# Optimization experiments

Hardware: AMD Instinct MI355X
Metric: run time of the kernel (lower is better)

Reference implementation:

```python
import jax, jax.numpy as jnp
import numpy as np

B, N, M, E = 2, 16384, 16384, 49152
W_CHAMFER, W_EDGE = 1.0, 0.1


def setup_inputs() -> dict:
    key = jax.random.key(0)
    k1, k2, k3 = jax.random.split(key, 3)
    pred_verts = jax.random.normal(k1, (B, N, 3), dtype=jnp.float32)
    target_verts = jax.random.normal(k2, (B, M, 3), dtype=jnp.float32)
    edges = jax.random.randint(k3, (E, 2), 0, N, dtype=jnp.int64)
    return {"pred_verts": pred_verts, "target_verts": target_verts, "edges": edges}


def reference(pred_verts, target_verts, edges):
    # --- Chamfer distance (torch.cdist + bidirectional min) ---
    # Squared-distance expansion avoids materializing the B x N x M x 3 diff tensor.
    p2 = jnp.sum(pred_verts * pred_verts, axis=-1)            # [B, N]
    t2 = jnp.sum(target_verts * target_verts, axis=-1)        # [B, M]
    cross = jnp.einsum('bnd,bmd->bnm', pred_verts, target_verts)  # [B, N, M]
    d2 = p2[:, :, None] + t2[:, None, :] - 2.0 * cross
    dist = jnp.sqrt(jnp.maximum(d2, 0.0))                     # [B, N, M]
    c_loss = jnp.mean(jnp.min(dist, axis=2)) + jnp.mean(jnp.min(dist, axis=1))

    # --- Edge-length variance regularization (vectorized over batch) ---
    v1 = pred_verts[:, edges[:, 0]]                           # [B, E, 3]
    v2 = pred_verts[:, edges[:, 1]]                           # [B, E, 3]
    edge_lengths = jnp.linalg.norm(v1 - v2, axis=-1)          # [B, E]
    # torch.var defaults to unbiased (ddof=1); mean over batch == sum/B
    e_loss = jnp.mean(jnp.var(edge_lengths, axis=1, ddof=1))

    total_loss = W_CHAMFER * c_loss + W_EDGE * e_loss
    return (total_loss, c_loss, e_loss)
```

## Files before the change

### kernel.cpp

```cpp
#include <hip/hip_runtime.h>
#include <float.h>

#define B_SZ 2
#define N_SZ 16384
#define E_SZ 49152

#define TPB 512
#define WAVES (TPB / 64)
#define ROWS_PER_BLOCK 128
#define NTILES (N_SZ / 32)
#define TILES_PER_CG (NTILES / 4)

#define CH_BLOCKS_PER_DIR (B_SZ * N_SZ / ROWS_PER_BLOCK)
#define CH_BLOCKS (2 * CH_BLOCKS_PER_DIR)
#define EDGE_BLOCKS (B_SZ * E_SZ / TPB)

#define PLANE_BYTES (N_SZ * 16)
#define BATCH_FRAG_BYTES (2 * PLANE_BYTES)
#define DIR_FRAG_BYTES (B_SZ * BATCH_FRAG_BYTES)
#define SUMS_OFF (2 * DIR_FRAG_BYTES)

typedef short short8 __attribute__((ext_vector_type(8)));
typedef float f32x16 __attribute__((ext_vector_type(16)));

__device__ inline short f2bf(float f) {
    unsigned u = __float_as_uint(f);
    unsigned r = (u + 0x7fffu + ((u >> 16) & 1u)) >> 16;
    return (short)r;
}
__device__ inline float bf2f(short s) {
    return __uint_as_float(((unsigned)(unsigned short)s) << 16);
}

__global__ __launch_bounds__(TPB) void prep(const float* __restrict__ pred,
                                            const float* __restrict__ tgt,
                                            char* __restrict__ ws) {
    int idx = blockIdx.x * TPB + threadIdx.x;
    double* sums = (double*)(ws + SUMS_OFF);
    if (blockIdx.x == 0 && threadIdx.x < 6) sums[threadIdx.x] = 0.0;

    const bool isTgt = idx < B_SZ * N_SZ;
    int row = isTgt ? idx : idx - B_SZ * N_SZ;
    int batch = row >> 14, pt = row & (N_SZ - 1);
    const float* src = (isTgt ? tgt : pred) + (size_t)row * 3;
    char* base = ws + (isTgt ? 0 : DIR_FRAG_BYTES) + (size_t)batch * BATCH_FRAG_BYTES;

    float tx = src[0], ty = src[1], tz = src[2];
    short hx = f2bf(tx), hy = f2bf(ty), hz = f2bf(tz);
    short lx = f2bf(tx - bf2f(hx)), ly = f2bf(ty - bf2f(hy)), lz = f2bf(tz - bf2f(hz));
    float t2 = fmaf(tx, tx, fmaf(ty, ty, tz * tz));
    short t2h = f2bf(t2), t2l = f2bf(t2 - bf2f(t2h));
    const short one = 0x3f80;

    *(short8*)(base + (size_t)pt * 16) = (short8){hx, hy, hz, hx, hy, hz, one, one};
    *(short8*)(base + PLANE_BYTES + (size_t)pt * 16) =
        (short8){lx, ly, lz, t2h, t2l, 0, 0, 0};
}

__global__ __launch_bounds__(TPB, 2) void main_kernel(
    const float* __restrict__ pred, const float* __restrict__ tgt,
    const int* __restrict__ edges, char* __restrict__ ws)
{
    __shared__ float wred[WAVES], wred2[WAVES];
    __shared__ int rowMin[ROWS_PER_BLOCK];
    double* sums = (double*)(ws + SUMS_OFF);
    const int lane = threadIdx.x & 63;
    const int wv = threadIdx.x >> 6;
    const int t = threadIdx.x;

    if (blockIdx.x < CH_BLOCKS) {
        const int dir = blockIdx.x >> 8;
        const int xb = blockIdx.x & 255;
        const int batch = xb >> 7;
        const int rowInB = (xb & 127) * ROWS_PER_BLOCK;
        const float* P = dir ? tgt : pred;
        const char* fragBase = ws + (size_t)dir * DIR_FRAG_BYTES
                                  + (size_t)batch * BATCH_FRAG_BYTES;
        const int bl = lane & 31;
        const int half = lane >> 5;
        const int rp = wv & 1;
        const int cg = wv >> 1;

        if (t < ROWS_PER_BLOCK) rowMin[t] = 0x7f7fffff;

        const short one = 0x3f80;
        short8 af[2];
        #pragma unroll
        for (int j = 0; j < 2; j++) {
            int r = batch * N_SZ + rowInB + rp * 64 + j * 32 + bl;
            const float* p = P + (size_t)r * 3;
            float px = p[0], py = p[1], pz = p[2];
            float ax = -2.f * px, ay = -2.f * py, az = -2.f * pz;
            short ahx = f2bf(ax), ahy = f2bf(ay), ahz = f2bf(az);
            short alx = f2bf(ax - bf2f(ahx)), aly = f2bf(ay - bf2f(ahy)),
                  alz = f2bf(az - bf2f(ahz));
            float p2 = fmaf(px, px, fmaf(py, py, pz * pz));
            short p2h = f2bf(p2), p2l = f2bf(p2 - bf2f(p2h));
            af[j] = half == 0
                ? (short8){ahx, ahy, ahz, alx, aly, alz, p2h, p2l}
                : (short8){ahx, ahy, ahz, one, one, 0, 0, 0};
        }

        float acc0[16], acc1[16];
        #pragma unroll
        for (int e = 0; e < 16; e++) { acc0[e] = FLT_MAX; acc1[e] = FLT_MAX; }
        const f32x16 zc = {0.f, 0.f, 0.f, 0.f, 0.f, 0.f, 0.f, 0.f,
                           0.f, 0.f, 0.f, 0.f, 0.f, 0.f, 0.f, 0.f};

        const char* bbase = fragBase + (size_t)half * PLANE_BYTES
                                     + (size_t)bl * 16;
        const int tbase = cg * TILES_PER_CG;
        auto ldb = [&](int tc) {
            return *(const short8*)(bbase + (size_t)tc * 512);
        };

        #define DOPAIR(X0, X1)                                                 \
            do {                                                               \
                f32x16 r0 = __builtin_amdgcn_mfma_f32_32x32x16_bf16(af[0], X0, zc, 0, 0, 0); \
                f32x16 r1 = __builtin_amdgcn_mfma_f32_32x32x16_bf16(af[0], X1, zc, 0, 0, 0); \
                _Pragma("unroll")                                              \
                for (int e = 0; e < 16; e++)                                   \
                    acc0[e] = fminf(fminf(r0[e], r1[e]), acc0[e]);             \
                f32x16 s0 = __builtin_amdgcn_mfma_f32_32x32x16_bf16(af[1], X0, zc, 0, 0, 0); \
                f32x16 s1 = __builtin_amdgcn_mfma_f32_32x32x16_bf16(af[1], X1, zc, 0, 0, 0); \
                _Pragma("unroll")                                              \
                for (int e = 0; e < 16; e++)                                   \
                    acc1[e] = fminf(fminf(s0[e], s1[e]), acc1[e]);             \
            } while (0)

        short8 b0 = ldb(tbase + 0), b1 = ldb(tbase + 1);
        short8 b2 = ldb(tbase + 2), b3 = ldb(tbase + 3);
        __syncthreads();

        #pragma unroll 1
        for (int i = 0; i < TILES_PER_CG / 4; i++) {
            int pf = (i < TILES_PER_CG / 4 - 1) ? tbase + 4 * (i + 1) : tbase;
            {
                short8 x0 = b0, x1 = b1;
                b0 = ldb(pf + 0); b1 = ldb(pf + 1);
                DOPAIR(x0, x1);
            }
            {
                short8 x0 = b2, x1 = b3;
                b2 = ldb(pf + 2); b3 = ldb(pf + 3);
                DOPAIR(x0, x1);
            }
        }

        #pragma unroll
        for (int j = 0; j < 2; j++) {
            #pragma unroll
            for (int e = 0; e < 16; e++) {
                float v = (j == 0) ? acc0[e] : acc1[e];
                v = fminf(v, __shfl_xor(v, 1));
                v = fminf(v, __shfl_xor(v, 2));
                v = fminf(v, __shfl_xor(v, 4));
                v = fminf(v, __shfl_xor(v, 8));
                v = fminf(v, __shfl_xor(v, 16));
                if (bl == 0) {
                    int row = rp * 64 + j * 32 + (e & 3) + 8 * (e >> 2) + 4 * half;
                    atomicMin(&rowMin[row], __float_as_int(fmaxf(v, 0.f)));
                }
            }
        }
        __syncthreads();

        if (t < ROWS_PER_BLOCK) {
            float s = sqrtf(__int_as_float(rowMin[t]));
            #pragma unroll
            for (int o = 32; o > 0; o >>= 1) s += __shfl_down(s, o, 64);
            if (lane == 0) wred[wv] = s;
        }
        __syncthreads();
        if (t == 0) atomicAdd(&sums[dir], (double)(wred[0] + wred[1]));
    } else {
        int idx = (blockIdx.x - CH_BLOCKS) * TPB + threadIdx.x;
        int b = idx >= E_SZ;
        int e = idx - b * E_SZ;
        int2 ee = ((const int2*)edges)[e];
        const float* p0 = pred + ((size_t)b * N_SZ + (size_t)ee.x) * 3;
        const float* p1 = pred + ((size_t)b * N_SZ + (size_t)ee.y) * 3;
        float dx = p0[0] - p1[0], dy = p0[1] - p1[1], dz = p0[2] - p1[2];
        float len = sqrtf(dx * dx + dy * dy + dz * dz);
        float s = len, q = len * len;
        for (int o = 32; o > 0; o >>= 1) {
            s += __shfl_down(s, o, 64);
            q += __shfl_down(q, o, 64);
        }
        if (lane == 0) { wred[wv] = s; wred2[wv] = q; }
        __syncthreads();
        if (threadIdx.x == 0) {
            float ts = 0.f, tq = 0.f;
            #pragma unroll
            for (int w = 0; w < WAVES; w++) { ts += wred[w]; tq += wred2[w]; }
            atomicAdd(&sums[2 + 2 * b], (double)ts);
            atomicAdd(&sums[3 + 2 * b], (double)tq);
        }
    }
}

__global__ void final_kernel(const char* __restrict__ ws, float* __restrict__ out) {
    const double* sums = (const double*)(ws + SUMS_OFF);
    double c = sums[0] / (double)(B_SZ * N_SZ) + sums[1] / (double)(B_SZ * N_SZ);
    double e = 0.0;
    #pragma unroll
    for (int b = 0; b < B_SZ; b++) {
        double s = sums[2 + 2 * b], q = sums[3 + 2 * b];
        e += (q - s * s / (double)E_SZ) / (double)(E_SZ - 1);
    }
    e *= (1.0 / B_SZ);
    double tot = 1.0 * c + 0.1 * e;
    out[0] = (float)tot;
    out[1] = (float)c;
    out[2] = (float)e;
}

extern "C" void kernel_launch(void* const* d_in, const int* in_sizes, int n_in,
                              void* d_out, int out_size, void* d_ws, size_t ws_size,
                              hipStream_t stream) {
    const float* pred = (const float*)d_in[0];
    const float* tgt  = (const float*)d_in[1];
    const int* edges  = (const int*)d_in[2];
    float* out = (float*)d_out;
    char* ws = (char*)d_ws;

    prep<<<dim3((2 * B_SZ * N_SZ) / TPB), TPB, 0, stream>>>(pred, tgt, ws);

    main_kernel<<<dim3(CH_BLOCKS + EDGE_BLOCKS), TPB, 0, stream>>>(
        pred, tgt, edges, ws);

    final_kernel<<<dim3(1), dim3(1), 0, stream>>>(ws, out);
}
```

Before: 104.0 us.

## Compute both chamfer directions from one distance pass with column-min reduction

Instead of running the distance matrix twice (pred→tgt and tgt→pred), each block now computes the pred×tgt tile once and derives both the row minima and the column minima. Column minima are reduced in a 64KB LDS array per block and then merged into a global array with atomicMin. A new colsum kernel takes sqrt of each column minimum and sums them. This halves the MFMA work, but adds per-tile shuffle and LDS atomic traffic, a large LDS footprint that may reduce occupancy, and global atomic merges.

```diff
diff --git a/kernel.cpp b/kernel.cpp
--- a/kernel.cpp
+++ b/kernel.cpp
@@ -11,13 +11,13 @@
 #define NTILES (N_SZ / 32)
 #define TILES_PER_CG (NTILES / 4)
 
-#define CH_BLOCKS_PER_DIR (B_SZ * N_SZ / ROWS_PER_BLOCK)
-#define CH_BLOCKS (2 * CH_BLOCKS_PER_DIR)
+#define CH_BLOCKS (B_SZ * N_SZ / ROWS_PER_BLOCK)
 #define EDGE_BLOCKS (B_SZ * E_SZ / TPB)
 
 #define PLANE_BYTES (N_SZ * 16)
 #define BATCH_FRAG_BYTES (2 * PLANE_BYTES)
 #define DIR_FRAG_BYTES (B_SZ * BATCH_FRAG_BYTES)
+#define COLMIN_OFF DIR_FRAG_BYTES
 #define SUMS_OFF (2 * DIR_FRAG_BYTES)
 
 typedef short short8 __attribute__((ext_vector_type(8)));
@@ -32,18 +32,16 @@
     return __uint_as_float(((unsigned)(unsigned short)s) << 16);
 }
 
-__global__ __launch_bounds__(TPB) void prep(const float* __restrict__ pred,
-                                            const float* __restrict__ tgt,
+__global__ __launch_bounds__(TPB) void prep(const float* __restrict__ tgt,
                                             char* __restrict__ ws) {
     int idx = blockIdx.x * TPB + threadIdx.x;
     double* sums = (double*)(ws + SUMS_OFF);
     if (blockIdx.x == 0 && threadIdx.x < 6) sums[threadIdx.x] = 0.0;
-
-    const bool isTgt = idx < B_SZ * N_SZ;
-    int row = isTgt ? idx : idx - B_SZ * N_SZ;
-    int batch = row >> 14, pt = row & (N_SZ - 1);
-    const float* src = (isTgt ? tgt : pred) + (size_t)row * 3;
-    char* base = ws + (isTgt ? 0 : DIR_FRAG_BYTES) + (size_t)batch * BATCH_FRAG_BYTES;
+    ((int*)(ws + COLMIN_OFF))[idx] = 0x7f7fffff;
+
+    int batch = idx >> 14, pt = idx & (N_SZ - 1);
+    const float* src = tgt + (size_t)idx * 3;
+    char* base = ws + (size_t)batch * BATCH_FRAG_BYTES;
 
     float tx = src[0], ty = src[1], tz = src[2];
     short hx = f2bf(tx), hy = f2bf(ty), hz = f2bf(tz);
@@ -61,6 +59,7 @@
     const float* __restrict__ pred, const float* __restrict__ tgt,
     const int* __restrict__ edges, char* __restrict__ ws)
 {
+    __shared__ int colLds[N_SZ];
     __shared__ float wred[WAVES], wred2[WAVES];
     __shared__ int rowMin[ROWS_PER_BLOCK];
     double* sums = (double*)(ws + SUMS_OFF);
@@ -69,18 +68,15 @@
     const int t = threadIdx.x;
 
     if (blockIdx.x < CH_BLOCKS) {
-        const int dir = blockIdx.x >> 8;
-        const int xb = blockIdx.x & 255;
-        const int batch = xb >> 7;
-        const int rowInB = (xb & 127) * ROWS_PER_BLOCK;
-        const float* P = dir ? tgt : pred;
-        const char* fragBase = ws + (size_t)dir * DIR_FRAG_BYTES
-                                  + (size_t)batch * BATCH_FRAG_BYTES;
+        const int batch = blockIdx.x >> 7;
+        const int rowInB = (blockIdx.x & 127) * ROWS_PER_BLOCK;
+        const char* fragBase = ws + (size_t)batch * BATCH_FRAG_BYTES;
         const int bl = lane & 31;
         const int half = lane >> 5;
         const int rp = wv & 1;
         const int cg = wv >> 1;
 
+        for (int k = t; k < N_SZ; k += TPB) colLds[k] = 0x7f7fffff;
         if (t < ROWS_PER_BLOCK) rowMin[t] = 0x7f7fffff;
 
         const short one = 0x3f80;
@@ -88,7 +84,7 @@
         #pragma unroll
         for (int j = 0; j < 2; j++) {
             int r = batch * N_SZ + rowInB + rp * 64 + j * 32 + bl;
-            const float* p = P + (size_t)r * 3;
+            const float* p = pred + (size_t)r * 3;
             float px = p[0], py = p[1], pz = p[2];
             float ax = -2.f * px, ay = -2.f * py, az = -2.f * pz;
             short ahx = f2bf(ax), ahy = f2bf(ay), ahz = f2bf(az);
@@ -113,20 +109,31 @@
         auto ldb = [&](int tc) {
             return *(const short8*)(bbase + (size_t)tc * 512);
         };
-
-        #define DOPAIR(X0, X1)                                                 \
-            do {                                                               \
-                f32x16 r0 = __builtin_amdgcn_mfma_f32_32x32x16_bf16(af[0], X0, zc, 0, 0, 0); \
-                f32x16 r1 = __builtin_amdgcn_mfma_f32_32x32x16_bf16(af[0], X1, zc, 0, 0, 0); \
-                _Pragma("unroll")                                              \
-                for (int e = 0; e < 16; e++)                                   \
-                    acc0[e] = fminf(fminf(r0[e], r1[e]), acc0[e]);             \
-                f32x16 s0 = __builtin_amdgcn_mfma_f32_32x32x16_bf16(af[1], X0, zc, 0, 0, 0); \
-                f32x16 s1 = __builtin_amdgcn_mfma_f32_32x32x16_bf16(af[1], X1, zc, 0, 0, 0); \
-                _Pragma("unroll")                                              \
-                for (int e = 0; e < 16; e++)                                   \
-                    acc1[e] = fminf(fminf(s0[e], s1[e]), acc1[e]);             \
-            } while (0)
+        auto coltree = [&](const f32x16& r, const f32x16& s, int tc) {
+            float m[8];
+            #pragma unroll
+            for (int e = 0; e < 8; e++)
+                m[e] = fminf(fminf(r[e], r[e + 8]), fminf(s[e], s[e + 8]));
+            float cv = fminf(fminf(fminf(m[0], m[1]), fminf(m[2], m[3])),
+                             fminf(fminf(m[4], m[5]), fminf(m[6], m[7])));
+            cv = fminf(cv, __shfl_xor(cv, 32));
+            if (half == 0)
+                atomicMin(&colLds[tc * 32 + bl], __float_as_int(fmaxf(cv, 0.f)));
+        };
+        auto dopair = [&](short8 x0, short8 x1, int tc0) {
+            f32x16 r0 = __builtin_amdgcn_mfma_f32_32x32x16_bf16(af[0], x0, zc, 0, 0, 0);
+            f32x16 r1 = __builtin_amdgcn_mfma_f32_32x32x16_bf16(af[0], x1, zc, 0, 0, 0);
+            f32x16 s0 = __builtin_amdgcn_mfma_f32_32x32x16_bf16(af[1], x0, zc, 0, 0, 0);
+            f32x16 s1 = __builtin_amdgcn_mfma_f32_32x32x16_bf16(af[1], x1, zc, 0, 0, 0);
+            #pragma unroll
+            for (int e = 0; e < 16; e++)
+                acc0[e] = fminf(fminf(r0[e], r1[e]), acc0[e]);
+            #pragma unroll
+            for (int e = 0; e < 16; e++)
+                acc1[e] = fminf(fminf(s0[e], s1[e]), acc1[e]);
+            coltree(r0, s0, tc0);
+            coltree(r1, s1, tc0 + 1);
+        };
 
         short8 b0 = ldb(tbase + 0), b1 = ldb(tbase + 1);
         short8 b2 = ldb(tbase + 2), b3 = ldb(tbase + 3);
@@ -134,16 +141,17 @@
 
         #pragma unroll 1
         for (int i = 0; i < TILES_PER_CG / 4; i++) {
-            int pf = (i < TILES_PER_CG / 4 - 1) ? tbase + 4 * (i + 1) : tbase;
+            int tc = tbase + 4 * i;
+            int pf = (i < TILES_PER_CG / 4 - 1) ? tc + 4 : tbase;
             {
                 short8 x0 = b0, x1 = b1;
                 b0 = ldb(pf + 0); b1 = ldb(pf + 1);
-                DOPAIR(x0, x1);
+                dopair(x0, x1, tc);
             }
             {
                 short8 x0 = b2, x1 = b3;
                 b2 = ldb(pf + 2); b3 = ldb(pf + 3);
-                DOPAIR(x0, x1);
+                dopair(x0, x1, tc + 2);
             }
         }
 
@@ -172,7 +180,13 @@
             if (lane == 0) wred[wv] = s;
         }
         __syncthreads();
-        if (t == 0) atomicAdd(&sums[dir], (double)(wred[0] + wred[1]));
+        if (t == 0) atomicAdd(&sums[0], (double)(wred[0] + wred[1]));
+
+        int* colG = (int*)(ws + COLMIN_OFF) + batch * N_SZ;
+        for (int k = t; k < N_SZ; k += TPB) {
+            int v = colLds[k];
+            if (v < colG[k]) atomicMin(&colG[k], v);
+        }
     } else {
         int idx = (blockIdx.x - CH_BLOCKS) * TPB + threadIdx.x;
         int b = idx >= E_SZ;
@@ -196,6 +210,24 @@
             atomicAdd(&sums[2 + 2 * b], (double)ts);
             atomicAdd(&sums[3 + 2 * b], (double)tq);
         }
+    }
+}
+
+__global__ __launch_bounds__(TPB) void colsum_kernel(char* __restrict__ ws) {
+    __shared__ float wr[WAVES];
+    const int* colG = (const int*)(ws + COLMIN_OFF);
+    double* sums = (double*)(ws + SUMS_OFF);
+    int idx = blockIdx.x * TPB + threadIdx.x;
+    float v = sqrtf(__int_as_float(colG[idx]));
+    #pragma unroll
+    for (int o = 32; o > 0; o >>= 1) v += __shfl_down(v, o, 64);
+    if ((threadIdx.x & 63) == 0) wr[threadIdx.x >> 6] = v;
+    __syncthreads();
+    if (threadIdx.x == 0) {
+        float s = 0.f;
+        #pragma unroll
+        for (int w = 0; w < WAVES; w++) s += wr[w];
+        atomicAdd(&sums[1], (double)s);
     }
 }
 
@@ -224,10 +256,12 @@
     float* out = (float*)d_out;
     char* ws = (char*)d_ws;
 
-    prep<<<dim3((2 * B_SZ * N_SZ) / TPB), TPB, 0, stream>>>(pred, tgt, ws);
+    prep<<<dim3((B_SZ * N_SZ) / TPB), TPB, 0, stream>>>(tgt, ws);
 
     main_kernel<<<dim3(CH_BLOCKS + EDGE_BLOCKS), TPB, 0, stream>>>(
         pred, tgt, edges, ws);
 
+    colsum_kernel<<<dim3((B_SZ * N_SZ) / TPB), TPB, 0, stream>>>(ws);
+
     final_kernel<<<dim3(1), dim3(1), 0, stream>>>(ws, out);
 }
```

Result: slower. 179.0 us (+72.1%).

## Software-pipeline MFMA results and deepen B-fragment prefetch in chamfer loop

Applied to the files above, without the earlier changes.

Restructures the chamfer inner loop so each step issues four MFMAs into one set of result registers while the min-reduction consumes the previous step's results. The aim is to hide MFMA latency behind the fminf work. The prefetch distance also grows from four to eight tiles, held in eight B registers, to better cover load latency. The cost is many more live vector registers, which can lower occupancy. The final prefetch also reads past each tile range, though those values are never used.

```diff
diff --git a/kernel.cpp b/kernel.cpp
--- a/kernel.cpp
+++ b/kernel.cpp
@@ -106,46 +106,60 @@
         for (int e = 0; e < 16; e++) { acc0[e] = FLT_MAX; acc1[e] = FLT_MAX; }
         const f32x16 zc = {0.f, 0.f, 0.f, 0.f, 0.f, 0.f, 0.f, 0.f,
                            0.f, 0.f, 0.f, 0.f, 0.f, 0.f, 0.f, 0.f};
+        const f32x16 fm = {FLT_MAX, FLT_MAX, FLT_MAX, FLT_MAX,
+                           FLT_MAX, FLT_MAX, FLT_MAX, FLT_MAX,
+                           FLT_MAX, FLT_MAX, FLT_MAX, FLT_MAX,
+                           FLT_MAX, FLT_MAX, FLT_MAX, FLT_MAX};
 
         const char* bbase = fragBase + (size_t)half * PLANE_BYTES
                                      + (size_t)bl * 16;
-        const int tbase = cg * TILES_PER_CG;
-        auto ldb = [&](int tc) {
-            return *(const short8*)(bbase + (size_t)tc * 512);
-        };
-
-        #define DOPAIR(X0, X1)                                                 \
+        const char* bp = bbase + (size_t)(cg * TILES_PER_CG) * 512;
+
+        short8 b0 = *(const short8*)(bp + 0 * 512);
+        short8 b1 = *(const short8*)(bp + 1 * 512);
+        short8 b2 = *(const short8*)(bp + 2 * 512);
+        short8 b3 = *(const short8*)(bp + 3 * 512);
+        short8 b4 = *(const short8*)(bp + 4 * 512);
+        short8 b5 = *(const short8*)(bp + 5 * 512);
+        short8 b6 = *(const short8*)(bp + 6 * 512);
+        short8 b7 = *(const short8*)(bp + 7 * 512);
+
+        f32x16 Ap0, Ap1, Aq0, Aq1;
+        f32x16 Bp0 = fm, Bp1 = fm, Bq0 = fm, Bq1 = fm;
+
+        #define STEP(BX0, BX1, CUR, PRV, PF)                                   \
             do {                                                               \
-                f32x16 r0 = __builtin_amdgcn_mfma_f32_32x32x16_bf16(af[0], X0, zc, 0, 0, 0); \
-                f32x16 r1 = __builtin_amdgcn_mfma_f32_32x32x16_bf16(af[0], X1, zc, 0, 0, 0); \
+                CUR##p0 = __builtin_amdgcn_mfma_f32_32x32x16_bf16(af[0], BX0, zc, 0, 0, 0); \
+                CUR##p1 = __builtin_amdgcn_mfma_f32_32x32x16_bf16(af[0], BX1, zc, 0, 0, 0); \
+                CUR##q0 = __builtin_amdgcn_mfma_f32_32x32x16_bf16(af[1], BX0, zc, 0, 0, 0); \
+                CUR##q1 = __builtin_amdgcn_mfma_f32_32x32x16_bf16(af[1], BX1, zc, 0, 0, 0); \
+                BX0 = *(const short8*)(bp + (PF) * 512);                       \
+                BX1 = *(const short8*)(bp + ((PF) + 1) * 512);                 \
                 _Pragma("unroll")                                              \
                 for (int e = 0; e < 16; e++)                                   \
-                    acc0[e] = fminf(fminf(r0[e], r1[e]), acc0[e]);             \
-                f32x16 s0 = __builtin_amdgcn_mfma_f32_32x32x16_bf16(af[1], X0, zc, 0, 0, 0); \
-                f32x16 s1 = __builtin_amdgcn_mfma_f32_32x32x16_bf16(af[1], X1, zc, 0, 0, 0); \
+                    acc0[e] = fminf(fminf(PRV##p0[e], PRV##p1[e]), acc0[e]);   \
                 _Pragma("unroll")                                              \
                 for (int e = 0; e < 16; e++)                                   \
-                    acc1[e] = fminf(fminf(s0[e], s1[e]), acc1[e]);             \
+                    acc1[e] = fminf(fminf(PRV##q0[e], PRV##q1[e]), acc1[e]);   \
             } while (0)
 
-        short8 b0 = ldb(tbase + 0), b1 = ldb(tbase + 1);
-        short8 b2 = ldb(tbase + 2), b3 = ldb(tbase + 3);
         __syncthreads();
 
         #pragma unroll 1
-        for (int i = 0; i < TILES_PER_CG / 4; i++) {
-            int pf = (i < TILES_PER_CG / 4 - 1) ? tbase + 4 * (i + 1) : tbase;
-            {
-                short8 x0 = b0, x1 = b1;
-                b0 = ldb(pf + 0); b1 = ldb(pf + 1);
-                DOPAIR(x0, x1);
-            }
-            {
-                short8 x0 = b2, x1 = b3;
-                b2 = ldb(pf + 2); b3 = ldb(pf + 3);
-                DOPAIR(x0, x1);
-            }
-        }
+        for (int i = 0; i < TILES_PER_CG / 8; i++) {
+            STEP(b0, b1, A, B, 8);
+            STEP(b2, b3, B, A, 10);
+            STEP(b4, b5, A, B, 12);
+            STEP(b6, b7, B, A, 14);
+            bp += 8 * 512;
+        }
+        #pragma unroll
+        for (int e = 0; e < 16; e++)
+            acc0[e] = fminf(fminf(Bp0[e], Bp1[e]), acc0[e]);
+        #pragma unroll
+        for (int e = 0; e < 16; e++)
+            acc1[e] = fminf(fminf(Bq0[e], Bq1[e]), acc1[e]);
+        #undef STEP
 
         #pragma unroll
         for (int j = 0; j < 2; j++) {
```

New measurement: 113.5 us. +9.2%, slower.
